# Performance work log

Measured on AMD Instinct MI355X. Metric: run time of the kernel, lower is better.

Reference implementation:

```python
import jax, jax.numpy as jnp
import numpy as np

N_NODES = 100000
N_EDGES = 1600000
IN_FEATS = 128
OUT_FEATS = 128
LN_EPS = 1e-5


def setup_inputs() -> dict:
    key = jax.random.key(0)
    k_h, k_w, k_b, k_src, k_dst = jax.random.split(key, 5)
    stdv = 1.0 / np.sqrt(OUT_FEATS)
    return {
        "h": jax.random.normal(k_h, (N_NODES, IN_FEATS), dtype=jnp.float32),
        "weight": jax.random.uniform(k_w, (IN_FEATS, OUT_FEATS), dtype=jnp.float32, minval=-stdv, maxval=stdv),
        "bias": jax.random.uniform(k_b, (OUT_FEATS,), dtype=jnp.float32, minval=-stdv, maxval=stdv),
        "gamma": jnp.ones((OUT_FEATS,), dtype=jnp.float32),
        "beta": jnp.zeros((OUT_FEATS,), dtype=jnp.float32),
        "src": jax.random.randint(k_src, (N_EDGES,), 0, N_NODES, dtype=jnp.int32),
        "dst": jax.random.randint(k_dst, (N_EDGES,), 0, N_NODES, dtype=jnp.int32),
    }


def reference(h, weight, bias, gamma, beta, src, dst):
    n = h.shape[0]
    # in-degree norm: 1/deg with inf -> 0 (isolated nodes)
    deg = jax.ops.segment_sum(jnp.ones_like(dst, dtype=h.dtype), dst, num_segments=n)
    norm = jnp.where(deg > 0, 1.0 / deg, 0.0)[:, None]  # [N, 1]
    # update_all(copy_src, sum): scatter-add of source features onto destinations
    ah = jax.ops.segment_sum(h[src], dst, num_segments=n)  # [N, in_feats]
    x = ah * norm
    x = x @ weight + bias  # [N, out_feats]
    # LayerNorm over feature dim with affine params
    mu = jnp.mean(x, axis=-1, keepdims=True)
    var = jnp.mean(jnp.square(x - mu), axis=-1, keepdims=True)
    x = (x - mu) * jax.lax.rsqrt(var + LN_EPS) * gamma + beta
    return jax.nn.relu(x)
```

## Files before the change

kernel.cpp:

```cpp
#include <hip/hip_runtime.h>

#define F 128
#define SCANB 1024
#define NBLK 256
#define BSHIFT 6
#define MAXNB 2048
#define SMEM_BYTES 43264

typedef __attribute__((ext_vector_type(8))) short short8;
typedef __attribute__((ext_vector_type(4))) float f32x4;

static __device__ __forceinline__ short f2bf(float f) {
    union { float f; unsigned u; } v; v.f = f;
    unsigned r = v.u + 0x7FFF + ((v.u >> 16) & 1);
    return (short)(r >> 16);
}
static __device__ __forceinline__ float bf_lo(unsigned u) {
    return __builtin_bit_cast(float, u << 16);
}
static __device__ __forceinline__ float bf_hi(unsigned u) {
    return __builtin_bit_cast(float, u & 0xFFFF0000u);
}
static __device__ __forceinline__ uint4 pack8(float a0,float a1,float a2,float a3,
                                              float a4,float a5,float a6,float a7) {
    uint4 o;
    o.x = ((unsigned)(unsigned short)f2bf(a1) << 16) | (unsigned short)f2bf(a0);
    o.y = ((unsigned)(unsigned short)f2bf(a3) << 16) | (unsigned short)f2bf(a2);
    o.z = ((unsigned)(unsigned short)f2bf(a5) << 16) | (unsigned short)f2bf(a4);
    o.w = ((unsigned)(unsigned short)f2bf(a7) << 16) | (unsigned short)f2bf(a6);
    return o;
}

__global__ __launch_bounds__(256) void k_gemm_hist(
    const float* __restrict__ h, const float* __restrict__ w,
    unsigned* __restrict__ hb, const int* __restrict__ dst,
    int* __restrict__ mat, int n_nodes, int n_edges, int nb, int hblk) {
    __shared__ alignas(16) char smem[SMEM_BYTES];
    const int tid = threadIdx.x;
    const int bid = blockIdx.x;

    if (bid < hblk) {
        int* lh = (int*)smem;
        for (int i = tid; i < nb; i += 256) lh[i] = 0;
        __syncthreads();
        const int epb = (n_edges + hblk - 1) / hblk;
        const int e0 = bid * epb, e1 = min(e0 + epb, n_edges);
        for (int e = e0 + tid; e < e1; e += 256)
            atomicAdd(&lh[dst[e] >> BSHIFT], 1);
        __syncthreads();
        for (int i = tid; i < nb; i += 256)
            mat[(size_t)i * NBLK + bid] = lh[i];
        return;
    }

    short* wt = (short*)smem;
    float* xs = (float*)(smem + 34816);
    {
        int n = tid & 127;
        for (int k = tid >> 7; k < 128; k += 2)
            wt[n * 136 + k] = f2bf(w[(size_t)k * 128 + n]);
    }
    __syncthreads();

    const int wv = tid >> 6, l = tid & 63, lr = l & 15, lk = l >> 4, q = l & 15;
    const int base = (bid - hblk) * 64;
    if (base >= n_nodes) return;
    const int row = base + wv * 16 + lr;
    const bool valid = row < n_nodes;

    short8 af[4];
    #pragma unroll
    for (int kk = 0; kk < 4; ++kk) {
        int k0 = kk * 32 + lk * 8;
        float4 a0{0,0,0,0}, a1{0,0,0,0};
        if (valid) {
            a0 = *(const float4*)(h + (size_t)row * F + k0);
            a1 = *(const float4*)(h + (size_t)row * F + k0 + 4);
        }
        af[kk] = short8{ f2bf(a0.x), f2bf(a0.y), f2bf(a0.z), f2bf(a0.w),
                         f2bf(a1.x), f2bf(a1.y), f2bf(a1.z), f2bf(a1.w) };
    }
    f32x4 acc[8];
    #pragma unroll
    for (int n = 0; n < 8; ++n) acc[n] = f32x4{0, 0, 0, 0};
    #pragma unroll
    for (int kk = 0; kk < 4; ++kk) {
        const int kb = kk * 32 + lk * 8;
        #pragma unroll
        for (int n = 0; n < 8; ++n) {
            short8 bfr = *(const short8*)(&wt[(n * 16 + lr) * 136 + kb]);
            acc[n] = __builtin_amdgcn_mfma_f32_16x16x32_bf16(af[kk], bfr, acc[n], 0, 0, 0);
        }
    }
    float* xw = xs + wv * (4 * 132);
    #pragma unroll
    for (int r = 0; r < 4; ++r) {
        #pragma unroll
        for (int n = 0; n < 8; ++n)
            xw[lk * 132 + n * 16 + lr] = acc[n][r];
        int grow = base + wv * 16 + lk * 4 + r;
        float4 a = *(const float4*)&xw[lk * 132 + q * 8];
        float4 b = *(const float4*)&xw[lk * 132 + q * 8 + 4];
        uint4 o = pack8(a.x, a.y, a.z, a.w, b.x, b.y, b.z, b.w);
        if (grow < n_nodes)
            ((uint4*)hb)[(size_t)grow * 16 + q] = o;
    }
}

__global__ __launch_bounds__(SCANB) void k_scan_a(const int* in, int* out,
                                                  int* bsum, int n) {
    __shared__ int tmp[SCANB];
    int i = blockIdx.x * SCANB + threadIdx.x;
    int v = (i < n) ? in[i] : 0;
    tmp[threadIdx.x] = v;
    __syncthreads();
    for (int off = 1; off < SCANB; off <<= 1) {
        int t = (threadIdx.x >= off) ? tmp[threadIdx.x - off] : 0;
        __syncthreads();
        tmp[threadIdx.x] += t;
        __syncthreads();
    }
    if (i < n) out[i] = tmp[threadIdx.x] - v;
    if (threadIdx.x == SCANB - 1) bsum[blockIdx.x] = tmp[SCANB - 1];
}

__global__ __launch_bounds__(512) void k_scan_b(int* bsum, int nb) {
    __shared__ int tmp[512];
    int i = threadIdx.x;
    int v = (i < nb) ? bsum[i] : 0;
    tmp[i] = v;
    __syncthreads();
    for (int off = 1; off < 512; off <<= 1) {
        int t = (i >= off) ? tmp[i - off] : 0;
        __syncthreads();
        tmp[i] += t;
        __syncthreads();
    }
    if (i < nb) bsum[i] = tmp[i] - v;
}

__global__ __launch_bounds__(SCANB) void k_scan_c(int* out, const int* bsum, int n) {
    int i = blockIdx.x * SCANB + threadIdx.x;
    if (i < n) out[i] += bsum[blockIdx.x];
}

__global__ __launch_bounds__(512) void k_part_scatter(
    const int* __restrict__ src, const int* __restrict__ dst,
    const int* __restrict__ mat, const int* __restrict__ bsum,
    unsigned* __restrict__ binned, int n_edges, int nb, int epb) {
    __shared__ int lbase[MAXNB];
    const int bid = blockIdx.x;
    for (int i = threadIdx.x; i < nb; i += 512) {
        int idx = i * NBLK + bid;
        lbase[i] = mat[idx] + bsum[idx >> 10];
    }
    __syncthreads();
    int e0 = bid * epb;
    int e1 = min(e0 + epb, n_edges);
    for (int e = e0 + threadIdx.x; e < e1; e += 512) {
        int d = dst[e];
        int b = d >> BSHIFT;
        int pos = atomicAdd(&lbase[b], 1);
        binned[pos] = ((unsigned)(d & ((1 << BSHIFT) - 1)) << 26) | (unsigned)src[e];
    }
}

__global__ __launch_bounds__(256) void k_bin_to_csr(
    const unsigned* __restrict__ binned, const int* __restrict__ mat,
    const int* __restrict__ bsum, int* __restrict__ deg, int* __restrict__ offs,
    int* __restrict__ esrc, int n_edges, int n_nodes, int nb) {
    __shared__ int ldeg[64], loffs[64], lcur[64];
    int b = blockIdx.x;
    int i0 = b * NBLK;
    int start = mat[i0] + bsum[i0 >> 10];
    int end = n_edges;
    if (b + 1 < nb) {
        int i1 = (b + 1) * NBLK;
        end = mat[i1] + bsum[i1 >> 10];
    }
    int cnt = end - start;
    int base_node = b << BSHIFT;
    int nn = min(1 << BSHIFT, n_nodes - base_node);
    for (int i = threadIdx.x; i < nn; i += 256) { ldeg[i] = 0; lcur[i] = 0; }
    __syncthreads();
    for (int i = threadIdx.x; i < cnt; i += 256)
        atomicAdd(&ldeg[binned[start + i] >> 26], 1);
    __syncthreads();
    if (threadIdx.x == 0) {
        int run = 0;
        for (int i = 0; i < nn; ++i) { loffs[i] = run; run += ldeg[i]; }
    }
    __syncthreads();
    for (int i = threadIdx.x; i < nn; i += 256) {
        deg[base_node + i]  = ldeg[i];
        offs[base_node + i] = start + loffs[i];
    }
    for (int i = threadIdx.x; i < cnt; i += 256) {
        unsigned p = binned[start + i];
        int ln = p >> 26;
        int pos = start + loffs[ln] + atomicAdd(&lcur[ln], 1);
        esrc[pos] = (int)(p & ((1u << 26) - 1));
    }
}

__global__ __launch_bounds__(256) void k_hist(const int* __restrict__ dst,
                                              int* __restrict__ deg, int n_edges) {
    int e = blockIdx.x * 256 + threadIdx.x;
    if (e < n_edges) atomicAdd(&deg[dst[e]], 1);
}

__global__ __launch_bounds__(256) void k_scatter_idx(
    const int* __restrict__ src, const int* __restrict__ dst,
    const int* __restrict__ offs, int* __restrict__ cursor,
    int* __restrict__ esrc, int n_edges) {
    int e = blockIdx.x * 256 + threadIdx.x;
    if (e >= n_edges) return;
    int d = dst[e];
    int pos = offs[d] + atomicAdd(&cursor[d], 1);
    esrc[pos] = src[e];
}

__global__ __launch_bounds__(256) void k_gather_ln(
    const unsigned* __restrict__ hb, const int* __restrict__ esrc,
    const int* __restrict__ offs, const int* __restrict__ deg,
    const float* __restrict__ bias, const float* __restrict__ gamma,
    const float* __restrict__ beta, float* __restrict__ out, int n_nodes) {
    int t = blockIdx.x * 256 + threadIdx.x;
    int node = t >> 6;
    int l = t & 63;
    if (node >= n_nodes) return;
    const int g = l >> 4;
    const int q = l & 15;

    const int start = offs[node];
    const int dn = deg[node];
    const int end = start + dn;

    float a0=0,a1=0,a2=0,a3=0,a4=0,a5=0,a6=0,a7=0;
    int i = start;
    for (; i + 16 <= end; i += 16) {
        int s0 = esrc[i + g];
        int s1 = esrc[i + 4 + g];
        int s2 = esrc[i + 8 + g];
        int s3 = esrc[i + 12 + g];
        uint4 v0 = *((const uint4*)(hb + (size_t)s0 * 64 + q * 4));
        uint4 v1 = *((const uint4*)(hb + (size_t)s1 * 64 + q * 4));
        uint4 v2 = *((const uint4*)(hb + (size_t)s2 * 64 + q * 4));
        uint4 v3 = *((const uint4*)(hb + (size_t)s3 * 64 + q * 4));
        a0 += (bf_lo(v0.x) + bf_lo(v1.x)) + (bf_lo(v2.x) + bf_lo(v3.x));
        a1 += (bf_hi(v0.x) + bf_hi(v1.x)) + (bf_hi(v2.x) + bf_hi(v3.x));
        a2 += (bf_lo(v0.y) + bf_lo(v1.y)) + (bf_lo(v2.y) + bf_lo(v3.y));
        a3 += (bf_hi(v0.y) + bf_hi(v1.y)) + (bf_hi(v2.y) + bf_hi(v3.y));
        a4 += (bf_lo(v0.z) + bf_lo(v1.z)) + (bf_lo(v2.z) + bf_lo(v3.z));
        a5 += (bf_hi(v0.z) + bf_hi(v1.z)) + (bf_hi(v2.z) + bf_hi(v3.z));
        a6 += (bf_lo(v0.w) + bf_lo(v1.w)) + (bf_lo(v2.w) + bf_lo(v3.w));
        a7 += (bf_hi(v0.w) + bf_hi(v1.w)) + (bf_hi(v2.w) + bf_hi(v3.w));
    }
    for (; i + 8 <= end; i += 8) {
        int s0 = esrc[i + g];
        int s1 = esrc[i + 4 + g];
        uint4 v0 = *((const uint4*)(hb + (size_t)s0 * 64 + q * 4));
        uint4 v1 = *((const uint4*)(hb + (size_t)s1 * 64 + q * 4));
        a0 += bf_lo(v0.x) + bf_lo(v1.x); a1 += bf_hi(v0.x) + bf_hi(v1.x);
        a2 += bf_lo(v0.y) + bf_lo(v1.y); a3 += bf_hi(v0.y) + bf_hi(v1.y);
        a4 += bf_lo(v0.z) + bf_lo(v1.z); a5 += bf_hi(v0.z) + bf_hi(v1.z);
        a6 += bf_lo(v0.w) + bf_lo(v1.w); a7 += bf_hi(v0.w) + bf_hi(v1.w);
    }
    for (; i < end; i += 4) {
        int e = i + g;
        if (e < end) {
            int s = esrc[e];
            uint4 v = *((const uint4*)(hb + (size_t)s * 64 + q * 4));
            a0 += bf_lo(v.x); a1 += bf_hi(v.x);
            a2 += bf_lo(v.y); a3 += bf_hi(v.y);
            a4 += bf_lo(v.z); a5 += bf_hi(v.z);
            a6 += bf_lo(v.w); a7 += bf_hi(v.w);
        }
    }
    #pragma unroll
    for (int m = 16; m <= 32; m <<= 1) {
        a0 += __shfl_xor(a0, m); a1 += __shfl_xor(a1, m);
        a2 += __shfl_xor(a2, m); a3 += __shfl_xor(a3, m);
        a4 += __shfl_xor(a4, m); a5 += __shfl_xor(a5, m);
        a6 += __shfl_xor(a6, m); a7 += __shfl_xor(a7, m);
    }
    float4 bs0 = *(const float4*)(bias  + q * 8);
    float4 bs1 = *(const float4*)(bias  + q * 8 + 4);
    const float nv = dn > 0 ? 1.0f / (float)dn : 0.0f;
    float f0 = a0 * nv + bs0.x, f1 = a1 * nv + bs0.y;
    float f2 = a2 * nv + bs0.z, f3 = a3 * nv + bs0.w;
    float f4 = a4 * nv + bs1.x, f5 = a5 * nv + bs1.y;
    float f6 = a6 * nv + bs1.z, f7 = a7 * nv + bs1.w;

    float s  = ((f0 + f1) + (f2 + f3)) + ((f4 + f5) + (f6 + f7));
    float q2 = ((f0*f0 + f1*f1) + (f2*f2 + f3*f3)) + ((f4*f4 + f5*f5) + (f6*f6 + f7*f7));
    #pragma unroll
    for (int m = 1; m <= 8; m <<= 1) {
        s  += __shfl_xor(s, m);
        q2 += __shfl_xor(q2, m);
    }
    float mu   = s * (1.0f / F);
    float var  = q2 * (1.0f / F) - mu * mu;
    float rstd = rsqrtf(var + 1e-5f);

    if (g == 0) {
        float4 gm0 = *(const float4*)(gamma + q * 8);
        float4 gm1 = *(const float4*)(gamma + q * 8 + 4);
        float4 bt0 = *(const float4*)(beta  + q * 8);
        float4 bt1 = *(const float4*)(beta  + q * 8 + 4);
        float4 o0, o1;
        o0.x = fmaxf((f0 - mu) * rstd * gm0.x + bt0.x, 0.0f);
        o0.y = fmaxf((f1 - mu) * rstd * gm0.y + bt0.y, 0.0f);
        o0.z = fmaxf((f2 - mu) * rstd * gm0.z + bt0.z, 0.0f);
        o0.w = fmaxf((f3 - mu) * rstd * gm0.w + bt0.w, 0.0f);
        o1.x = fmaxf((f4 - mu) * rstd * gm1.x + bt1.x, 0.0f);
        o1.y = fmaxf((f5 - mu) * rstd * gm1.y + bt1.y, 0.0f);
        o1.z = fmaxf((f6 - mu) * rstd * gm1.z + bt1.z, 0.0f);
        o1.w = fmaxf((f7 - mu) * rstd * gm1.w + bt1.w, 0.0f);
        float* op = out + (size_t)node * F + q * 8;
        *(float4*)op = o0;
        *(float4*)(op + 4) = o1;
    }
}

extern "C" void kernel_launch(void* const* d_in, const int* in_sizes, int n_in,
                              void* d_out, int out_size, void* d_ws, size_t ws_size,
                              hipStream_t stream) {
    const float* h      = (const float*)d_in[0];
    const float* weight = (const float*)d_in[1];
    const float* bias   = (const float*)d_in[2];
    const float* gamma  = (const float*)d_in[3];
    const float* beta   = (const float*)d_in[4];
    const int*   src    = (const int*)d_in[5];
    const int*   dst    = (const int*)d_in[6];

    const int n_nodes = in_sizes[0] / F;
    const int n_edges = in_sizes[5];

    float* x = (float*)d_out;

    const int nb = (n_nodes + (1 << BSHIFT) - 1) >> BSHIFT;
    const int len = nb * NBLK;
    const int nscan = (len + SCANB - 1) / SCANB;
    const bool shift_ok = (nb <= MAXNB) && (nscan <= 512) && (n_nodes <= (1 << 26));

    int* deg    = (int*)d_ws;
    int* offs   = deg + n_nodes;
    int* esrc   = offs + n_nodes;
    unsigned* hb = (unsigned*)(esrc + n_edges);
    int* bsum   = (int*)(hb + (size_t)n_nodes * 64);
    int* mat    = bsum + 1024;
    unsigned* binned = (unsigned*)(mat + (size_t)len);
    int* cursor = mat;

    size_t need_common = ((size_t)2 * n_nodes + (size_t)n_edges + 1024) * sizeof(int)
                       + (size_t)n_nodes * 64 * sizeof(unsigned);
    size_t need_new  = need_common + ((size_t)len + (size_t)n_edges) * sizeof(int);
    size_t need_fall = need_common + (size_t)n_nodes * sizeof(int);
    bool use_new = shift_ok && ws_size >= need_new;

    const int gb = (n_nodes + 63) / 64;

    if (use_new) {
        k_gemm_hist<<<NBLK + gb, 256, 0, stream>>>(h, weight, hb, dst, mat,
                                                   n_nodes, n_edges, nb, NBLK);
        k_scan_a<<<nscan, SCANB, 0, stream>>>(mat, mat, bsum, len);
        k_scan_b<<<1, 512, 0, stream>>>(bsum, nscan);
        const int epb = (n_edges + NBLK - 1) / NBLK;
        k_part_scatter<<<NBLK, 512, 0, stream>>>(src, dst, mat, bsum, binned,
                                                 n_edges, nb, epb);
        k_bin_to_csr<<<nb, 256, 0, stream>>>(binned, mat, bsum, deg, offs, esrc,
                                             n_edges, n_nodes, nb);
        int gblocks = (int)(((size_t)n_nodes * 64 + 255) / 256);
        k_gather_ln<<<gblocks, 256, 0, stream>>>(hb, esrc, offs, deg,
                                                 bias, gamma, beta, x, n_nodes);
    } else if (ws_size >= need_fall) {
        k_gemm_hist<<<gb, 256, 0, stream>>>(h, weight, hb, dst, mat,
                                            n_nodes, n_edges, nb, 0);
        const int nscan2 = (n_nodes + SCANB - 1) / SCANB;
        hipMemsetAsync(deg, 0, (size_t)n_nodes * sizeof(int), stream);
        hipMemsetAsync(cursor, 0, (size_t)n_nodes * sizeof(int), stream);
        k_hist<<<(n_edges + 255) / 256, 256, 0, stream>>>(dst, deg, n_edges);
        k_scan_a<<<nscan2, SCANB, 0, stream>>>(deg, offs, bsum, n_nodes);
        k_scan_b<<<1, 512, 0, stream>>>(bsum, nscan2);
        k_scan_c<<<nscan2, SCANB, 0, stream>>>(offs, bsum, n_nodes);
        k_scatter_idx<<<(n_edges + 255) / 256, 256, 0, stream>>>(
            src, dst, offs, cursor, esrc, n_edges);
        int gblocks = (int)(((size_t)n_nodes * 64 + 255) / 256);
        k_gather_ln<<<gblocks, 256, 0, stream>>>(hb, esrc, offs, deg,
                                                 bias, gamma, beta, x, n_nodes);
    }
}
```

Baseline: 132.8 us.

## Store projected features as fp16, accumulate gathers with packed half2, widen bins

The projected node features are now packed as fp16 instead of bf16, and the neighbor gather accumulates with packed half2 adds instead of unpacking each element to fp32. This cuts the ALU work in the gather loop. The binning partition is widened to 128 nodes per bin, which halves the number of bins, scan entries and CSR-build blocks. The risk is fp16 range and precision loss, since summing many neighbors in half precision can lose accuracy or overflow.

```diff
diff --git a/kernel.cpp b/kernel.cpp
--- a/kernel.cpp
+++ b/kernel.cpp
@@ -1,9 +1,10 @@
 #include <hip/hip_runtime.h>
+#include <hip/hip_fp16.h>
 
 #define F 128
 #define SCANB 1024
 #define NBLK 256
-#define BSHIFT 6
+#define BSHIFT 7
 #define MAXNB 2048
 #define SMEM_BYTES 43264
 
@@ -15,19 +16,16 @@
     unsigned r = v.u + 0x7FFF + ((v.u >> 16) & 1);
     return (short)(r >> 16);
 }
-static __device__ __forceinline__ float bf_lo(unsigned u) {
-    return __builtin_bit_cast(float, u << 16);
-}
-static __device__ __forceinline__ float bf_hi(unsigned u) {
-    return __builtin_bit_cast(float, u & 0xFFFF0000u);
-}
-static __device__ __forceinline__ uint4 pack8(float a0,float a1,float a2,float a3,
-                                              float a4,float a5,float a6,float a7) {
+static __device__ __forceinline__ __half2 h2(unsigned u) {
+    return __builtin_bit_cast(__half2, u);
+}
+static __device__ __forceinline__ uint4 pack8h(float a0,float a1,float a2,float a3,
+                                               float a4,float a5,float a6,float a7) {
     uint4 o;
-    o.x = ((unsigned)(unsigned short)f2bf(a1) << 16) | (unsigned short)f2bf(a0);
-    o.y = ((unsigned)(unsigned short)f2bf(a3) << 16) | (unsigned short)f2bf(a2);
-    o.z = ((unsigned)(unsigned short)f2bf(a5) << 16) | (unsigned short)f2bf(a4);
-    o.w = ((unsigned)(unsigned short)f2bf(a7) << 16) | (unsigned short)f2bf(a6);
+    o.x = __builtin_bit_cast(unsigned, __floats2half2_rn(a0, a1));
+    o.y = __builtin_bit_cast(unsigned, __floats2half2_rn(a2, a3));
+    o.z = __builtin_bit_cast(unsigned, __floats2half2_rn(a4, a5));
+    o.w = __builtin_bit_cast(unsigned, __floats2half2_rn(a6, a7));
     return o;
 }
 
@@ -101,7 +99,7 @@
         int grow = base + wv * 16 + lk * 4 + r;
         float4 a = *(const float4*)&xw[lk * 132 + q * 8];
         float4 b = *(const float4*)&xw[lk * 132 + q * 8 + 4];
-        uint4 o = pack8(a.x, a.y, a.z, a.w, b.x, b.y, b.z, b.w);
+        uint4 o = pack8h(a.x, a.y, a.z, a.w, b.x, b.y, b.z, b.w);
         if (grow < n_nodes)
             ((uint4*)hb)[(size_t)grow * 16 + q] = o;
     }
@@ -161,7 +159,7 @@
         int d = dst[e];
         int b = d >> BSHIFT;
         int pos = atomicAdd(&lbase[b], 1);
-        binned[pos] = ((unsigned)(d & ((1 << BSHIFT) - 1)) << 26) | (unsigned)src[e];
+        binned[pos] = ((unsigned)(d & ((1 << BSHIFT) - 1)) << 25) | (unsigned)src[e];
     }
 }
 
@@ -169,7 +167,7 @@
     const unsigned* __restrict__ binned, const int* __restrict__ mat,
     const int* __restrict__ bsum, int* __restrict__ deg, int* __restrict__ offs,
     int* __restrict__ esrc, int n_edges, int n_nodes, int nb) {
-    __shared__ int ldeg[64], loffs[64], lcur[64];
+    __shared__ int ldeg[128], loffs[128], lcur[128];
     int b = blockIdx.x;
     int i0 = b * NBLK;
     int start = mat[i0] + bsum[i0 >> 10];
@@ -184,7 +182,7 @@
     for (int i = threadIdx.x; i < nn; i += 256) { ldeg[i] = 0; lcur[i] = 0; }
     __syncthreads();
     for (int i = threadIdx.x; i < cnt; i += 256)
-        atomicAdd(&ldeg[binned[start + i] >> 26], 1);
+        atomicAdd(&ldeg[binned[start + i] >> 25], 1);
     __syncthreads();
     if (threadIdx.x == 0) {
         int run = 0;
@@ -197,9 +195,9 @@
     }
     for (int i = threadIdx.x; i < cnt; i += 256) {
         unsigned p = binned[start + i];
-        int ln = p >> 26;
+        int ln = p >> 25;
         int pos = start + loffs[ln] + atomicAdd(&lcur[ln], 1);
-        esrc[pos] = (int)(p & ((1u << 26) - 1));
+        esrc[pos] = (int)(p & ((1u << 25) - 1));
     }
 }
 
@@ -236,7 +234,8 @@
     const int dn = deg[node];
     const int end = start + dn;
 
-    float a0=0,a1=0,a2=0,a3=0,a4=0,a5=0,a6=0,a7=0;
+    __half2 c0 = __floats2half2_rn(0.f, 0.f);
+    __half2 c1 = c0, c2 = c0, c3 = c0;
     int i = start;
     for (; i + 16 <= end; i += 16) {
         int s0 = esrc[i + g];
@@ -247,36 +246,37 @@
         uint4 v1 = *((const uint4*)(hb + (size_t)s1 * 64 + q * 4));
         uint4 v2 = *((const uint4*)(hb + (size_t)s2 * 64 + q * 4));
         uint4 v3 = *((const uint4*)(hb + (size_t)s3 * 64 + q * 4));
-        a0 += (bf_lo(v0.x) + bf_lo(v1.x)) + (bf_lo(v2.x) + bf_lo(v3.x));
-        a1 += (bf_hi(v0.x) + bf_hi(v1.x)) + (bf_hi(v2.x) + bf_hi(v3.x));
-        a2 += (bf_lo(v0.y) + bf_lo(v1.y)) + (bf_lo(v2.y) + bf_lo(v3.y));
-        a3 += (bf_hi(v0.y) + bf_hi(v1.y)) + (bf_hi(v2.y) + bf_hi(v3.y));
-        a4 += (bf_lo(v0.z) + bf_lo(v1.z)) + (bf_lo(v2.z) + bf_lo(v3.z));
-        a5 += (bf_hi(v0.z) + bf_hi(v1.z)) + (bf_hi(v2.z) + bf_hi(v3.z));
-        a6 += (bf_lo(v0.w) + bf_lo(v1.w)) + (bf_lo(v2.w) + bf_lo(v3.w));
-        a7 += (bf_hi(v0.w) + bf_hi(v1.w)) + (bf_hi(v2.w) + bf_hi(v3.w));
+        c0 = __hadd2(c0, __hadd2(__hadd2(h2(v0.x), h2(v1.x)), __hadd2(h2(v2.x), h2(v3.x))));
+        c1 = __hadd2(c1, __hadd2(__hadd2(h2(v0.y), h2(v1.y)), __hadd2(h2(v2.y), h2(v3.y))));
+        c2 = __hadd2(c2, __hadd2(__hadd2(h2(v0.z), h2(v1.z)), __hadd2(h2(v2.z), h2(v3.z))));
+        c3 = __hadd2(c3, __hadd2(__hadd2(h2(v0.w), h2(v1.w)), __hadd2(h2(v2.w), h2(v3.w))));
     }
     for (; i + 8 <= end; i += 8) {
         int s0 = esrc[i + g];
         int s1 = esrc[i + 4 + g];
         uint4 v0 = *((const uint4*)(hb + (size_t)s0 * 64 + q * 4));
         uint4 v1 = *((const uint4*)(hb + (size_t)s1 * 64 + q * 4));
-        a0 += bf_lo(v0.x) + bf_lo(v1.x); a1 += bf_hi(v0.x) + bf_hi(v1.x);
-        a2 += bf_lo(v0.y) + bf_lo(v1.y); a3 += bf_hi(v0.y) + bf_hi(v1.y);
-        a4 += bf_lo(v0.z) + bf_lo(v1.z); a5 += bf_hi(v0.z) + bf_hi(v1.z);
-        a6 += bf_lo(v0.w) + bf_lo(v1.w); a7 += bf_hi(v0.w) + bf_hi(v1.w);
+        c0 = __hadd2(c0, __hadd2(h2(v0.x), h2(v1.x)));
+        c1 = __hadd2(c1, __hadd2(h2(v0.y), h2(v1.y)));
+        c2 = __hadd2(c2, __hadd2(h2(v0.z), h2(v1.z)));
+        c3 = __hadd2(c3, __hadd2(h2(v0.w), h2(v1.w)));
     }
     for (; i < end; i += 4) {
         int e = i + g;
         if (e < end) {
             int s = esrc[e];
             uint4 v = *((const uint4*)(hb + (size_t)s * 64 + q * 4));
-            a0 += bf_lo(v.x); a1 += bf_hi(v.x);
-            a2 += bf_lo(v.y); a3 += bf_hi(v.y);
-            a4 += bf_lo(v.z); a5 += bf_hi(v.z);
-            a6 += bf_lo(v.w); a7 += bf_hi(v.w);
+            c0 = __hadd2(c0, h2(v.x));
+            c1 = __hadd2(c1, h2(v.y));
+            c2 = __hadd2(c2, h2(v.z));
+            c3 = __hadd2(c3, h2(v.w));
         }
     }
+    float2 p0 = __half22float2(c0), p1 = __half22float2(c1);
+    float2 p2 = __half22float2(c2), p3 = __half22float2(c3);
+    float a0 = p0.x, a1 = p0.y, a2 = p1.x, a3 = p1.y;
+    float a4 = p2.x, a5 = p2.y, a6 = p3.x, a7 = p3.y;
+
     #pragma unroll
     for (int m = 16; m <= 32; m <<= 1) {
         a0 += __shfl_xor(a0, m); a1 += __shfl_xor(a1, m);
@@ -342,7 +342,7 @@
     const int nb = (n_nodes + (1 << BSHIFT) - 1) >> BSHIFT;
     const int len = nb * NBLK;
     const int nscan = (len + SCANB - 1) / SCANB;
-    const bool shift_ok = (nb <= MAXNB) && (nscan <= 512) && (n_nodes <= (1 << 26));
+    const bool shift_ok = (nb <= MAXNB) && (nscan <= 512) && (n_nodes <= (1 << 25));
 
     int* deg    = (int*)d_ws;
     int* offs   = deg + n_nodes;
```

Result: faster. 129.6 us (-2.5%).
